# Performance work log

Hardware: AMD Instinct MI355X
Metric: run time of the kernel (lower is better)

## Reference

```python
import jax, jax.numpy as jnp
import numpy as np
from math import isqrt

NUM_HEADS = 8
EPS = 1e-12  # torch F.normalize default eps


def _l2_normalize_seq(t):
    # normalize over the sequence axis (dim=-2), matching F.normalize(t, dim=-2)
    n = jnp.sqrt(jnp.sum(t * t, axis=-2, keepdims=True))
    return t / jnp.maximum(n, EPS)


def setup_inputs() -> dict:
    key = jax.random.key(0)
    ks = jax.random.split(key, 7)
    B, L, C = 8, 4096, 384
    s = 0.02
    return {
        "x": jax.random.normal(ks[0], (B, L, C), jnp.float32),
        "qkv_w": jax.random.normal(ks[1], (3 * C, C), jnp.float32) * s,
        "qkv_b": jax.random.normal(ks[2], (3 * C,), jnp.float32) * s,
        "proj_w": jax.random.normal(ks[3], (C, C), jnp.float32) * s,
        "proj_b": jax.random.normal(ks[4], (C,), jnp.float32) * s,
        "temperature": jnp.ones((NUM_HEADS, 1, 1), jnp.float32),
        "conv_w": jax.random.normal(ks[5], (C, 1, 3, 3), jnp.float32) * s,
        "conv_b": jax.random.normal(ks[6], (C,), jnp.float32) * s,
    }


def reference(x, qkv_w, qkv_b, proj_w, proj_b, temperature, conv_w, conv_b):
    B, L, C = x.shape
    h = NUM_HEADS
    d = C // h
    H = W = isqrt(L)

    # qkv projection -> (3, B, h, L, d)
    qkv = (x @ qkv_w.T + qkv_b).reshape(B, L, 3, h, d).transpose(2, 0, 3, 1, 4)
    q, k, v = qkv[0], qkv[1], qkv[2]

    # L2 normalize q, k over sequence axis
    q = _l2_normalize_seq(q)
    k = _l2_normalize_seq(k)

    # LePE: depthwise 3x3 conv on v in image layout (B, C, H, W)
    v_img = v.transpose(0, 1, 3, 2).reshape(B, C, H, W)
    lepe = jax.lax.conv_general_dilated(
        v_img, conv_w, window_strides=(1, 1), padding=((1, 1), (1, 1)),
        feature_group_count=C,
        dimension_numbers=("NCHW", "OIHW", "NCHW"),
    ) + conv_b[None, :, None, None]
    lepe = lepe.reshape(B, h, d, L).transpose(0, 1, 3, 2)  # (B, h, L, d)

    # linear attention: attn = (k^T v) * temperature, shape (B, h, d, d)
    attn = jnp.einsum("bhld,bhle->bhde", k, v) * temperature
    out = jnp.einsum("bhld,bhde->bhle", q, attn) + lepe  # (B, h, L, d)

    out = out.transpose(0, 2, 1, 3).reshape(B, L, C)
    out = out @ proj_w.T + proj_b
    return (out, attn)
```

## Files before the change

kernel.cpp:

```cpp
#include <hip/hip_runtime.h>
#include <hip/hip_bf16.h>


typedef __bf16 bf16x8 __attribute__((ext_vector_type(8)));
typedef float f32x4 __attribute__((ext_vector_type(4)));

__device__ inline __bf16 f2b(float f) {
    __hip_bfloat16 h = __float2bfloat16(f);
    __bf16 r; __builtin_memcpy(&r, &h, 2); return r;
}
__device__ inline float b2f(__hip_bfloat16 h) { return __bfloat162float(h); }
__device__ inline float b2f(__bf16 v) {
    __hip_bfloat16 h; __builtin_memcpy(&h, &v, 2); return __bfloat162float(h);
}

__device__ inline bf16x8 load8(const __hip_bfloat16* p) {
    uint4 v = *(const uint4*)p;
    bf16x8 r; __builtin_memcpy(&r, &v, 16); return r;
}
__device__ inline bf16x8 load8(const float* p) {
    float4 a = *(const float4*)p;
    float4 b = *(const float4*)(p + 4);
    bf16x8 r;
    r[0] = f2b(a.x); r[1] = f2b(a.y); r[2] = f2b(a.z); r[3] = f2b(a.w);
    r[4] = f2b(b.x); r[5] = f2b(b.y); r[6] = f2b(b.z); r[7] = f2b(b.w);
    return r;
}

__device__ inline void storef(float* p, float v) { *p = v; }
__device__ inline void storef(__hip_bfloat16* p, float v) { *p = __float2bfloat16(v); }

__device__ inline void gl_lds16(const __hip_bfloat16* g, __hip_bfloat16* l) {
    __builtin_amdgcn_global_load_lds(
        (const __attribute__((address_space(1))) void*)g,
        (__attribute__((address_space(3))) void*)l,
        16, 0, 0);
}

__global__ __launch_bounds__(256) void cvt_kernel(
    const float* __restrict__ x,  __hip_bfloat16* __restrict__ xb,
    const float* __restrict__ qw, __hip_bfloat16* __restrict__ qwb,
    const float* __restrict__ pw, __hip_bfloat16* __restrict__ pwb,
    uint4* __restrict__ zdst)
{
    int blk = blockIdx.x;
    if (blk >= 6432) {
        zdst[(size_t)(blk - 6432) * 256 + threadIdx.x] = (uint4){0, 0, 0, 0};
        return;
    }
    const float* src; __hip_bfloat16* dst; int base;
    if (blk < 6144)      { src = x;  dst = xb;  base = blk; }
    else if (blk < 6360) { src = qw; dst = qwb; base = blk - 6144; }
    else                 { src = pw; dst = pwb; base = blk - 6360; }
    int i = base * 256 + threadIdx.x;
    bf16x8 v = load8(src + (size_t)i * 8);
    *(bf16x8*)(dst + (size_t)i * 8) = v;
}

template <typename TO, int KC, bool FUSE_SQ>
__global__ __launch_bounds__(256) void gemm_bf16_nt(
    const __hip_bfloat16* __restrict__ A,
    const __hip_bfloat16* __restrict__ Bw,
    const float* __restrict__ bias,
    TO* __restrict__ C,
    int N, int NXT,
    float* __restrict__ sq)
{
    __shared__ __hip_bfloat16 As[128 * 64];
    __shared__ __hip_bfloat16 Bs[64 * 64];
    const int t = threadIdx.x;
    const int w = t >> 6, lane = t & 63;
    const int r16 = lane & 15, quad = lane >> 4;
    const int bx  = blockIdx.x;
    const int xcd = bx & 7, seq = bx >> 3;
    const int n_t = seq % NXT, m_t = seq / NXT;
    const int m0 = (xcd + 8 * m_t) * 128;
    const int n0 = n_t * 64;
    const int wm = w >> 1, wn = w & 1;

    f32x4 acc[4][2];
    #pragma unroll
    for (int mi = 0; mi < 4; ++mi)
        #pragma unroll
        for (int ni = 0; ni < 2; ++ni)
            acc[mi][ni] = (f32x4){0.f, 0.f, 0.f, 0.f};

    for (int k0 = 0; k0 < KC; k0 += 64) {
        #pragma unroll
        for (int p = 0; p < 4; ++p) {
            int c = p * 64 + lane;
            int rl = c >> 3;
            int cc = (c & 7) ^ (rl & 7);
            gl_lds16(A + (size_t)(m0 + w * 32 + rl) * KC + k0 + cc * 8,
                     &As[(w * 256 + c) * 8]);
        }
        #pragma unroll
        for (int p = 0; p < 2; ++p) {
            int c = p * 64 + lane;
            int rl = c >> 3;
            int cc = (c & 7) ^ (rl & 7);
            gl_lds16(Bw + (size_t)(n0 + w * 16 + rl) * KC + k0 + cc * 8,
                     &Bs[(w * 128 + c) * 8]);
        }
        __syncthreads();
        bf16x8 af[4][2], bfr[2][2];
        #pragma unroll
        for (int ks = 0; ks < 2; ++ks) {
            #pragma unroll
            for (int mi = 0; mi < 4; ++mi) {
                int row = wm * 64 + mi * 16 + r16;
                int pc  = (ks * 4 + quad) ^ (r16 & 7);
                af[mi][ks] = *(const bf16x8*)&As[row * 64 + pc * 8];
            }
            #pragma unroll
            for (int ni = 0; ni < 2; ++ni) {
                int row = wn * 32 + ni * 16 + r16;
                int pc  = (ks * 4 + quad) ^ (r16 & 7);
                bfr[ni][ks] = *(const bf16x8*)&Bs[row * 64 + pc * 8];
            }
        }
        #pragma unroll
        for (int ks = 0; ks < 2; ++ks)
            #pragma unroll
            for (int mi = 0; mi < 4; ++mi)
                #pragma unroll
                for (int ni = 0; ni < 2; ++ni)
                    acc[mi][ni] = __builtin_amdgcn_mfma_f32_16x16x32_bf16(
                        af[mi][ks], bfr[ni][ks], acc[mi][ni], 0, 0, 0);
        __syncthreads();
    }

    #pragma unroll
    for (int ni = 0; ni < 2; ++ni) {
        int col = n0 + wn * 32 + ni * 16 + r16;
        float bv = bias[col];
        float s = 0.f;
        #pragma unroll
        for (int mi = 0; mi < 4; ++mi) {
            #pragma unroll
            for (int reg = 0; reg < 4; ++reg) {
                int row = m0 + wm * 64 + mi * 16 + quad * 4 + reg;
                float o = acc[mi][ni][reg] + bv;
                storef(&C[(size_t)row * N + col], o);
                s += o * o;
            }
        }
        if constexpr (FUSE_SQ) {
            if (col < 768) {
                s += __shfl_xor(s, 16);
                s += __shfl_xor(s, 32);
                if (quad == 0) {
                    int b = m0 >> 12;
                    atomicAdd(&sq[b * 768 + col], s);
                }
            }
        }
    }
}

__global__ __launch_bounds__(256) void ktv_mfma_kernel(
    const __hip_bfloat16* __restrict__ qkv, float* __restrict__ G)
{
    __shared__ __hip_bfloat16 kT[4][48][40];
    __shared__ __hip_bfloat16 vT[4][48][40];

    const int bh = blockIdx.y; const int b = bh >> 3; const int h = bh & 7;
    const int lbase = blockIdx.x * 256;
    const int t = threadIdx.x;
    const int w = t >> 6, lane = t & 63;
    const int r16 = lane & 15, quad = lane >> 4;

    f32x4 acc[3][3];
    #pragma unroll
    for (int mi = 0; mi < 3; ++mi)
        #pragma unroll
        for (int ni = 0; ni < 3; ++ni)
            acc[mi][ni] = (f32x4){0.f, 0.f, 0.f, 0.f};

    const int mat  = t & 1;
    const int lrow = t >> 1;
    const int tile = lrow >> 5, l_in = lrow & 31;
    const __hip_bfloat16* src = qkv + 384 + mat * 384 + h * 48;
    __hip_bfloat16* dstT = (mat ? &vT[0][0][0] : &kT[0][0][0]) + ((size_t)tile * 48 * 40 + l_in);

    for (int it = 0; it < 2; ++it) {
        const int l0 = lbase + it * 128;
        const __hip_bfloat16* p = src + (size_t)(b * 4096 + l0 + lrow) * 1152;
        __hip_bfloat16 row[48];
        #pragma unroll
        for (int j = 0; j < 6; ++j) {
            uint4 v = *(const uint4*)(p + j * 8);
            __builtin_memcpy(&row[j * 8], &v, 16);
        }
        #pragma unroll
        for (int d = 0; d < 48; ++d)
            dstT[d * 40] = row[d];
        __syncthreads();

        bf16x8 af[3], bfr[3];
        #pragma unroll
        for (int mi = 0; mi < 3; ++mi)
            af[mi] = *(const bf16x8*)&kT[w][mi * 16 + r16][quad * 8];
        #pragma unroll
        for (int ni = 0; ni < 3; ++ni)
            bfr[ni] = *(const bf16x8*)&vT[w][ni * 16 + r16][quad * 8];
        #pragma unroll
        for (int mi = 0; mi < 3; ++mi)
            #pragma unroll
            for (int ni = 0; ni < 3; ++ni)
                acc[mi][ni] = __builtin_amdgcn_mfma_f32_16x16x32_bf16(af[mi], bfr[ni], acc[mi][ni], 0, 0, 0);
        __syncthreads();
    }

    float* red2 = (float*)&kT[0][0][0];
    if (w >= 2) {
        #pragma unroll
        for (int mi = 0; mi < 3; ++mi)
            #pragma unroll
            for (int ni = 0; ni < 3; ++ni)
                #pragma unroll
                for (int reg = 0; reg < 4; ++reg)
                    red2[((w - 2) * 48 + mi * 16 + quad * 4 + reg) * 49 + ni * 16 + r16]
                        = acc[mi][ni][reg];
    }
    __syncthreads();
    if (w < 2) {
        float* Gb = G + (size_t)bh * 2304;
        #pragma unroll
        for (int mi = 0; mi < 3; ++mi)
            #pragma unroll
            for (int ni = 0; ni < 3; ++ni)
                #pragma unroll
                for (int reg = 0; reg < 4; ++reg) {
                    int row = mi * 16 + quad * 4 + reg;
                    int col = ni * 16 + r16;
                    float s = acc[mi][ni][reg] + red2[(w * 48 + row) * 49 + col];
                    atomicAdd(&Gb[row * 48 + col], s);
                }
    }
}

__global__ __launch_bounds__(256) void qattn_lepe_mfma(
    const __hip_bfloat16* __restrict__ qkv, const float* __restrict__ G,
    const float* __restrict__ sumsq, const float* __restrict__ temp,
    const float* __restrict__ conv_w, const float* __restrict__ conv_b,
    __hip_bfloat16* __restrict__ y, float* __restrict__ attn_out)
{
    __shared__ __attribute__((aligned(16))) char smem[26624];
    __hip_bfloat16 (*qs)[72]  = (__hip_bfloat16 (*)[72])smem;
    __hip_bfloat16 (*a2s)[72] = (__hip_bfloat16 (*)[72])(smem + 18432);
    float (*ys)[52]           = (float (*)[52])smem;
    __shared__ __hip_bfloat16 vs[4][64][48];
    __shared__ float cwT[9][48];
    __shared__ float cb[48];
    __shared__ float ink_s[48], inq_s[48];

    const int bh = blockIdx.y; const int b = bh >> 3; const int h = bh & 7;
    const int yi0 = blockIdx.x * 2;
    const int l0  = yi0 * 64;
    const int t = threadIdx.x;
    const int w = t >> 6, lane = t & 63;
    const int r16 = lane & 15, quad = lane >> 4;
    const float tf = temp[h];

    if (t < 48) {
        ink_s[t] = 1.f / fmaxf(sqrtf(sumsq[b * 768 + 384 + h * 48 + t]), 1e-12f);
        inq_s[t] = 1.f / fmaxf(sqrtf(sumsq[b * 768 +       h * 48 + t]), 1e-12f);
    }
    __syncthreads();

    const float* Gb = G + (size_t)bh * 2304;

    if (blockIdx.x == 0) {
        for (int e = t; e < 2304; e += 256)
            attn_out[(size_t)bh * 2304 + e] = Gb[e] * ink_s[e / 48] * tf;
    }

    const __hip_bfloat16* qbase = qkv + (size_t)(b * 4096 + l0) * 1152 + h * 48;
    #pragma unroll
    for (int i = 0; i < 3; ++i) {
        int chunk = t + i * 256;
        int row = chunk / 6, cg = chunk % 6;
        *(bf16x8*)&qs[row][cg * 8] = load8(qbase + (size_t)row * 1152 + cg * 8);
    }
    *(bf16x8*)&qs[t >> 1][48 + (t & 1) * 8] = (bf16x8)0;

    for (int i = t; i < 3072; i += 256) {
        int e = i >> 6, dd = i & 63;
        float val = 0.f;
        if (dd < 48) {
            float av = Gb[dd * 48 + e] * ink_s[dd] * tf;
            val = av * inq_s[dd];
        }
        a2s[e][dd] = __float2bfloat16(val);
    }

    const __hip_bfloat16* vbase = qkv + (size_t)b * 4096 * 1152 + 768 + h * 48;
    #pragma unroll
    for (int i = 0; i < 6; ++i) {
        int chunk = t + i * 256;
        int r = chunk / 384, rem = chunk % 384;
        int xx = rem / 6, cg = rem % 6;
        int yy = yi0 - 1 + r;
        bf16x8 v = (yy >= 0 && yy < 64)
            ? load8(vbase + (size_t)(yy * 64 + xx) * 1152 + cg * 8)
            : (bf16x8)0;
        *(bf16x8*)&vs[r][xx][cg * 8] = v;
    }

    for (int i = t; i < 432; i += 256)
        cwT[i / 48][i % 48] = conv_w[(h * 48 + (i % 48)) * 9 + (i / 48)];
    if (t < 48) cb[t] = conv_b[h * 48 + t];
    __syncthreads();

    f32x4 acc[2][3];
    #pragma unroll
    for (int mi = 0; mi < 2; ++mi)
        #pragma unroll
        for (int ni = 0; ni < 3; ++ni)
            acc[mi][ni] = (f32x4){0.f, 0.f, 0.f, 0.f};
    #pragma unroll
    for (int ks = 0; ks < 2; ++ks) {
        int kb = ks * 32 + quad * 8;
        bf16x8 af[2], bfr[3];
        #pragma unroll
        for (int mi = 0; mi < 2; ++mi)
            af[mi] = *(const bf16x8*)&qs[w * 32 + mi * 16 + r16][kb];
        #pragma unroll
        for (int ni = 0; ni < 3; ++ni)
            bfr[ni] = *(const bf16x8*)&a2s[ni * 16 + r16][kb];
        #pragma unroll
        for (int mi = 0; mi < 2; ++mi)
            #pragma unroll
            for (int ni = 0; ni < 3; ++ni)
                acc[mi][ni] = __builtin_amdgcn_mfma_f32_16x16x32_bf16(af[mi], bfr[ni], acc[mi][ni], 0, 0, 0);
    }
    __syncthreads();

    #pragma unroll
    for (int mi = 0; mi < 2; ++mi)
        #pragma unroll
        for (int ni = 0; ni < 3; ++ni)
            #pragma unroll
            for (int reg = 0; reg < 4; ++reg)
                ys[w * 32 + mi * 16 + quad * 4 + reg][ni * 16 + r16] = acc[mi][ni][reg];
    __syncthreads();

    __hip_bfloat16* ybase = y + (size_t)(b * 4096 + l0) * 384 + h * 48;
    #pragma unroll
    for (int i = 0; i < 3; ++i) {
        int g = t + i * 256;
        int l_in = g / 6, cg = g % 6, e0 = cg * 8;
        int xi = l_in & 63, vr0 = l_in >> 6;
        float o[8];
        #pragma unroll
        for (int j = 0; j < 8; ++j) o[j] = ys[l_in][e0 + j] + cb[e0 + j];
        #pragma unroll
        for (int dy = 0; dy < 3; ++dy) {
            #pragma unroll
            for (int dx = 0; dx < 3; ++dx) {
                int xx = xi + dx - 1;
                if (xx < 0 || xx > 63) continue;
                bf16x8 vv = *(const bf16x8*)&vs[vr0 + dy][xx][e0];
                const float* cwp = &cwT[dy * 3 + dx][e0];
                #pragma unroll
                for (int j = 0; j < 8; ++j) o[j] += b2f(vv[j]) * cwp[j];
            }
        }
        __hip_bfloat16 ob[8];
        #pragma unroll
        for (int j = 0; j < 8; ++j) ob[j] = __float2bfloat16(o[j]);
        uint4 pk; __builtin_memcpy(&pk, ob, 16);
        *(uint4*)(ybase + (size_t)l_in * 384 + e0) = pk;
    }
}

extern "C" void kernel_launch(void* const* d_in, const int* in_sizes, int n_in,
                              void* d_out, int out_size, void* d_ws, size_t ws_size,
                              hipStream_t stream)
{
    const float* x      = (const float*)d_in[0];
    const float* qkv_w  = (const float*)d_in[1];
    const float* qkv_b  = (const float*)d_in[2];
    const float* proj_w = (const float*)d_in[3];
    const float* proj_b = (const float*)d_in[4];
    const float* temp   = (const float*)d_in[5];
    const float* conv_w = (const float*)d_in[6];
    const float* conv_b = (const float*)d_in[7];

    char* ws = (char*)d_ws;
    __hip_bfloat16* qkv = (__hip_bfloat16*)(ws);
    __hip_bfloat16* yb  = (__hip_bfloat16*)(ws + 75497472);
    float* sumsq = (float*)(ws + 100663296);
    float* G     = (float*)(ws + 100687872);
    __hip_bfloat16* x_bf16  = yb;
    __hip_bfloat16* qkv_wb  = (__hip_bfloat16*)(ws + 101892096);
    __hip_bfloat16* proj_wb = (__hip_bfloat16*)(ws + 102776832);

    float* out      = (float*)d_out;
    float* attn_out = out + 12582912;

    cvt_kernel<<<6582, 256, 0, stream>>>(x, x_bf16, qkv_w, qkv_wb, proj_w, proj_wb,
                                         (uint4*)(ws + 100663296));
    gemm_bf16_nt<__hip_bfloat16, 384, true><<<4608, 256, 0, stream>>>(
        x_bf16, qkv_wb, qkv_b, qkv, 1152, 18, sumsq);
    ktv_mfma_kernel<<<dim3(16, 64), 256, 0, stream>>>(qkv, G);
    qattn_lepe_mfma<<<dim3(32, 64), 256, 0, stream>>>(
        qkv, G, sumsq, temp, conv_w, conv_b, yb, attn_out);
    gemm_bf16_nt<float, 384, false><<<1536, 256, 0, stream>>>(
        yb, proj_wb, proj_b, out, 384, 6, nullptr);
}
```

Before: 227.2 us.

## Restructure linear attention via per-batch Gram matrix and folded effective weights

```diff
diff --git a/kernel.cpp b/kernel.cpp
--- a/kernel.cpp
+++ b/kernel.cpp
@@ -57,14 +57,499 @@
     *(bf16x8*)(dst + (size_t)i * 8) = v;
 }
 
-template <typename TO, int KC, bool FUSE_SQ>
+__global__ __launch_bounds__(256) void xpose_kernel(
+    const __hip_bfloat16* __restrict__ xb, __hip_bfloat16* __restrict__ xT,
+    float* __restrict__ m)
+{
+    __shared__ __hip_bfloat16 tile[64][72];
+    const int lt = blockIdx.x, ct = blockIdx.y, b = blockIdx.z;
+    const int l0 = lt * 64, c0 = ct * 64;
+    const int t = threadIdx.x;
+
+    #pragma unroll
+    for (int p = 0; p < 2; ++p) {
+        int cid = t + p * 256;
+        int row = cid >> 3, ch = cid & 7;
+        *(bf16x8*)&tile[row][ch * 8] =
+            load8(xb + (size_t)(b * 4096 + l0 + row) * 384 + c0 + ch * 8);
+    }
+    __syncthreads();
+
+    #pragma unroll
+    for (int p = 0; p < 2; ++p) {
+        int ocid = t + p * 256;
+        int c = ocid >> 3, lch = ocid & 7;
+        __hip_bfloat16 vals[8];
+        #pragma unroll
+        for (int k = 0; k < 8; ++k) {
+            int j = (k + lch) & 7;
+            vals[j] = tile[lch * 8 + j][c];
+        }
+        bf16x8 pk;
+        float s = 0.f;
+        #pragma unroll
+        for (int j = 0; j < 8; ++j) { pk[j] = *(__bf16*)&vals[j]; s += b2f(vals[j]); }
+        *(bf16x8*)(xT + ((size_t)b * 384 + c0 + c) * 4096 + l0 + lch * 8) = pk;
+        s += __shfl_xor(s, 1); s += __shfl_xor(s, 2); s += __shfl_xor(s, 4);
+        if ((ocid & 7) == 0) atomicAdd(&m[b * 384 + c0 + c], s);
+    }
+}
+
+__global__ __launch_bounds__(256) void syrk_part(
+    const __hip_bfloat16* __restrict__ xT, float* __restrict__ Spart)
+{
+    __shared__ __hip_bfloat16 As[128 * 64];
+    __shared__ __hip_bfloat16 Bs[64 * 64];
+    const int t = threadIdx.x;
+    const int w = t >> 6, lane = t & 63;
+    const int r16 = lane & 15, quad = lane >> 4;
+    const int bx = blockIdx.x;
+    const int b = bx / 72, rem = bx % 72;
+    const int tile = rem / 4, split = rem % 4;
+    const int m0 = (tile / 6) * 128, n0 = (tile % 6) * 64;
+    const int k_lo = split * 1024;
+    const int wm = w >> 1, wn = w & 1;
+    const __hip_bfloat16* A = xT + (size_t)b * 384 * 4096;
+
+    f32x4 acc[4][2];
+    #pragma unroll
+    for (int mi = 0; mi < 4; ++mi)
+        #pragma unroll
+        for (int ni = 0; ni < 2; ++ni)
+            acc[mi][ni] = (f32x4){0.f, 0.f, 0.f, 0.f};
+
+    for (int it = 0; it < 16; ++it) {
+        const int k0 = k_lo + it * 64;
+        #pragma unroll
+        for (int p = 0; p < 4; ++p) {
+            int c = p * 64 + lane;
+            int rl = c >> 3;
+            int cc = (c & 7) ^ (rl & 7);
+            gl_lds16(A + (size_t)(m0 + w * 32 + rl) * 4096 + k0 + cc * 8,
+                     &As[(w * 256 + c) * 8]);
+        }
+        #pragma unroll
+        for (int p = 0; p < 2; ++p) {
+            int c = p * 64 + lane;
+            int rl = c >> 3;
+            int cc = (c & 7) ^ (rl & 7);
+            gl_lds16(A + (size_t)(n0 + w * 16 + rl) * 4096 + k0 + cc * 8,
+                     &Bs[(w * 128 + c) * 8]);
+        }
+        __syncthreads();
+        bf16x8 af[4][2], bfr[2][2];
+        #pragma unroll
+        for (int ks = 0; ks < 2; ++ks) {
+            #pragma unroll
+            for (int mi = 0; mi < 4; ++mi) {
+                int row = wm * 64 + mi * 16 + r16;
+                int pc  = (ks * 4 + quad) ^ (r16 & 7);
+                af[mi][ks] = *(const bf16x8*)&As[row * 64 + pc * 8];
+            }
+            #pragma unroll
+            for (int ni = 0; ni < 2; ++ni) {
+                int row = wn * 32 + ni * 16 + r16;
+                int pc  = (ks * 4 + quad) ^ (r16 & 7);
+                bfr[ni][ks] = *(const bf16x8*)&Bs[row * 64 + pc * 8];
+            }
+        }
+        #pragma unroll
+        for (int ks = 0; ks < 2; ++ks)
+            #pragma unroll
+            for (int mi = 0; mi < 4; ++mi)
+                #pragma unroll
+                for (int ni = 0; ni < 2; ++ni)
+                    acc[mi][ni] = __builtin_amdgcn_mfma_f32_16x16x32_bf16(
+                        af[mi][ks], bfr[ni][ks], acc[mi][ni], 0, 0, 0);
+        __syncthreads();
+    }
+
+    float* outp = Spart + (size_t)(split * 8 + b) * 147456;
+    #pragma unroll
+    for (int ni = 0; ni < 2; ++ni) {
+        int col = n0 + wn * 32 + ni * 16 + r16;
+        #pragma unroll
+        for (int mi = 0; mi < 4; ++mi)
+            #pragma unroll
+            for (int reg = 0; reg < 4; ++reg) {
+                int row = m0 + wm * 64 + mi * 16 + quad * 4 + reg;
+                outp[(size_t)row * 384 + col] = acc[mi][ni][reg];
+            }
+    }
+}
+
+__global__ __launch_bounds__(256) void cvtS_kernel(
+    const float* __restrict__ Spart, __hip_bfloat16* __restrict__ S2)
+{
+    size_t base = ((size_t)blockIdx.x * 256 + threadIdx.x) * 8;
+    int b = (int)(base / 147456);
+    size_t off = base % 147456;
+    float s[8];
+    #pragma unroll
+    for (int j = 0; j < 8; ++j) s[j] = 0.f;
+    #pragma unroll
+    for (int sp = 0; sp < 4; ++sp) {
+        const float* p = Spart + (size_t)(sp * 8 + b) * 147456 + off;
+        float4 a = *(const float4*)p, c = *(const float4*)(p + 4);
+        s[0] += a.x; s[1] += a.y; s[2] += a.z; s[3] += a.w;
+        s[4] += c.x; s[5] += c.y; s[6] += c.z; s[7] += c.w;
+    }
+    bf16x8 hi, lo;
+    #pragma unroll
+    for (int j = 0; j < 8; ++j) {
+        __hip_bfloat16 h = __float2bfloat16(s[j]);
+        hi[j] = *(__bf16*)&h;
+        __hip_bfloat16 l2 = __float2bfloat16(s[j] - __bfloat162float(h));
+        lo[j] = *(__bf16*)&l2;
+    }
+    *(bf16x8*)(S2 + (size_t)(b * 2 + 0) * 147456 + off) = hi;
+    *(bf16x8*)(S2 + (size_t)(b * 2 + 1) * 147456 + off) = lo;
+}
+
+__global__ __launch_bounds__(256) void gemm_T(
+    const __hip_bfloat16* __restrict__ Wqk, const __hip_bfloat16* __restrict__ S2,
+    float* __restrict__ T)
+{
+    __shared__ __hip_bfloat16 As[128 * 64];
+    __shared__ __hip_bfloat16 Bs[64 * 64];
+    const int t = threadIdx.x;
+    const int w = t >> 6, lane = t & 63;
+    const int r16 = lane & 15, quad = lane >> 4;
+    const int bx = blockIdx.x;
+    const int b = bx / 36, rem = bx % 36;
+    const int m0 = (rem / 6) * 128, n0 = (rem % 6) * 64;
+    const int wm = w >> 1, wn = w & 1;
+
+    f32x4 acc[4][2];
+    #pragma unroll
+    for (int mi = 0; mi < 4; ++mi)
+        #pragma unroll
+        for (int ni = 0; ni < 2; ++ni)
+            acc[mi][ni] = (f32x4){0.f, 0.f, 0.f, 0.f};
+
+    for (int pass = 0; pass < 2; ++pass) {
+        const __hip_bfloat16* Bw = S2 + (size_t)(b * 2 + pass) * 147456;
+        for (int k0 = 0; k0 < 384; k0 += 64) {
+            #pragma unroll
+            for (int p = 0; p < 4; ++p) {
+                int c = p * 64 + lane;
+                int rl = c >> 3;
+                int cc = (c & 7) ^ (rl & 7);
+                gl_lds16(Wqk + (size_t)(m0 + w * 32 + rl) * 384 + k0 + cc * 8,
+                         &As[(w * 256 + c) * 8]);
+            }
+            #pragma unroll
+            for (int p = 0; p < 2; ++p) {
+                int c = p * 64 + lane;
+                int rl = c >> 3;
+                int cc = (c & 7) ^ (rl & 7);
+                gl_lds16(Bw + (size_t)(n0 + w * 16 + rl) * 384 + k0 + cc * 8,
+                         &Bs[(w * 128 + c) * 8]);
+            }
+            __syncthreads();
+            bf16x8 af[4][2], bfr[2][2];
+            #pragma unroll
+            for (int ks = 0; ks < 2; ++ks) {
+                #pragma unroll
+                for (int mi = 0; mi < 4; ++mi) {
+                    int row = wm * 64 + mi * 16 + r16;
+                    int pc  = (ks * 4 + quad) ^ (r16 & 7);
+                    af[mi][ks] = *(const bf16x8*)&As[row * 64 + pc * 8];
+                }
+                #pragma unroll
+                for (int ni = 0; ni < 2; ++ni) {
+                    int row = wn * 32 + ni * 16 + r16;
+                    int pc  = (ks * 4 + quad) ^ (r16 & 7);
+                    bfr[ni][ks] = *(const bf16x8*)&Bs[row * 64 + pc * 8];
+                }
+            }
+            #pragma unroll
+            for (int ks = 0; ks < 2; ++ks)
+                #pragma unroll
+                for (int mi = 0; mi < 4; ++mi)
+                    #pragma unroll
+                    for (int ni = 0; ni < 2; ++ni)
+                        acc[mi][ni] = __builtin_amdgcn_mfma_f32_16x16x32_bf16(
+                            af[mi][ks], bfr[ni][ks], acc[mi][ni], 0, 0, 0);
+            __syncthreads();
+        }
+    }
+
+    float* Cp = T + (size_t)b * 768 * 384;
+    #pragma unroll
+    for (int ni = 0; ni < 2; ++ni) {
+        int col = n0 + wn * 32 + ni * 16 + r16;
+        #pragma unroll
+        for (int mi = 0; mi < 4; ++mi)
+            #pragma unroll
+            for (int reg = 0; reg < 4; ++reg) {
+                int row = m0 + wm * 64 + mi * 16 + quad * 4 + reg;
+                Cp[(size_t)row * 384 + col] = acc[mi][ni][reg];
+            }
+    }
+}
+
+__global__ __launch_bounds__(256) void head_kernel(
+    const float* __restrict__ T, const float* __restrict__ m,
+    const __hip_bfloat16* __restrict__ qkvw, const float* __restrict__ qkv_b,
+    const float* __restrict__ temp,
+    float* __restrict__ attn_out, __hip_bfloat16* __restrict__ weff,
+    float* __restrict__ beff)
+{
+    __shared__ __hip_bfloat16 wlds[48][384];
+    __shared__ float A2[48][48];
+    __shared__ float ink[48], inq[48], kbm[48], vbm[48], qbm[48];
+    __shared__ float bk_s[48], bv_s[48], bq_s[48];
+
+    const int bh = blockIdx.x; const int b = bh >> 3, h = bh & 7;
+    const int t = threadIdx.x;
+    const float tf = temp[h];
+    const float* mb = m + b * 384;
+    const float* tq = T + ((size_t)b * 768 + h * 48) * 384;
+    const float* tk = T + ((size_t)b * 768 + 384 + h * 48) * 384;
+
+    for (int i = t; i < 48 * 48; i += 256) {
+        int r = i / 48, c = i % 48;
+        *(bf16x8*)&wlds[r][c * 8] = load8(qkvw + (size_t)(768 + h * 48 + r) * 384 + c * 8);
+    }
+    if (t < 48) {
+        bq_s[t] = qkv_b[h * 48 + t];
+        bk_s[t] = qkv_b[384 + h * 48 + t];
+        bv_s[t] = qkv_b[768 + h * 48 + t];
+    }
+    if (t < 144) {
+        int kind = t / 48, d = t % 48;
+        int rbase = (kind == 0) ? 384 + h * 48 + d : (kind == 1) ? 768 + h * 48 + d : h * 48 + d;
+        const __hip_bfloat16* wr = qkvw + (size_t)rbase * 384;
+        float s = 0.f;
+        for (int j0 = 0; j0 < 384; j0 += 8) {
+            bf16x8 wv = load8(wr + j0);
+            const float4 a = *(const float4*)(mb + j0);
+            const float4 c = *(const float4*)(mb + j0 + 4);
+            s += b2f(wv[0])*a.x + b2f(wv[1])*a.y + b2f(wv[2])*a.z + b2f(wv[3])*a.w
+               + b2f(wv[4])*c.x + b2f(wv[5])*c.y + b2f(wv[6])*c.z + b2f(wv[7])*c.w;
+        }
+        if (kind == 0) kbm[d] = s; else if (kind == 1) vbm[d] = s; else qbm[d] = s;
+    }
+    __syncthreads();
+
+    if (t < 96) {
+        int d = t % 48; bool isq = t >= 48;
+        const float* trow = (isq ? tq : tk) + (size_t)d * 384;
+        const __hip_bfloat16* wr = qkvw + (size_t)((isq ? 0 : 384) + h * 48 + d) * 384;
+        float bb = isq ? bq_s[d] : bk_s[d];
+        float s = 0.f;
+        for (int j0 = 0; j0 < 384; j0 += 8) {
+            bf16x8 wv = load8(wr + j0);
+            const float4 a = *(const float4*)(trow + j0);
+            const float4 c = *(const float4*)(trow + j0 + 4);
+            s += a.x*b2f(wv[0]) + a.y*b2f(wv[1]) + a.z*b2f(wv[2]) + a.w*b2f(wv[3])
+               + c.x*b2f(wv[4]) + c.y*b2f(wv[5]) + c.z*b2f(wv[6]) + c.w*b2f(wv[7]);
+        }
+        s += 2.f * bb * (isq ? qbm[d] : kbm[d]) + 4096.f * bb * bb;
+        float r = 1.f / fmaxf(sqrtf(s), 1e-12f);
+        if (isq) inq[d] = r; else ink[d] = r;
+    }
+    __syncthreads();
+
+    #pragma unroll
+    for (int kk = 0; kk < 9; ++kk) {
+        int cell = t + kk * 256;
+        int d = cell / 48, e = cell % 48;
+        const float* trow = tk + (size_t)d * 384;
+        float g = 0.f;
+        for (int j0 = 0; j0 < 384; j0 += 8) {
+            bf16x8 wv = *(const bf16x8*)&wlds[e][j0];
+            const float4 a = *(const float4*)(trow + j0);
+            const float4 c = *(const float4*)(trow + j0 + 4);
+            g += a.x*b2f(wv[0]) + a.y*b2f(wv[1]) + a.z*b2f(wv[2]) + a.w*b2f(wv[3])
+               + c.x*b2f(wv[4]) + c.y*b2f(wv[5]) + c.z*b2f(wv[6]) + c.w*b2f(wv[7]);
+        }
+        g += kbm[d] * bv_s[e] + bk_s[d] * vbm[e] + 4096.f * bk_s[d] * bv_s[e];
+        float av = g * ink[d] * tf;
+        attn_out[(size_t)bh * 2304 + cell] = av;
+        A2[d][e] = av * inq[d];
+    }
+    __syncthreads();
+
+    for (int i = t; i < 48 * 48; i += 256) {
+        int r = i / 48, c = i % 48;
+        *(bf16x8*)&wlds[r][c * 8] = load8(qkvw + (size_t)(h * 48 + r) * 384 + c * 8);
+    }
+    if (t < 48) {
+        float s = 0.f;
+        #pragma unroll
+        for (int d2 = 0; d2 < 48; ++d2) s += bq_s[d2] * A2[d2][t];
+        beff[(size_t)b * 384 + h * 48 + t] = s;
+    }
+    __syncthreads();
+
+    for (int idx = t; idx < 48 * 384; idx += 256) {
+        int e = idx / 384, i2 = idx % 384;
+        float s = 0.f;
+        #pragma unroll
+        for (int d2 = 0; d2 < 48; ++d2) s += A2[d2][e] * b2f(wlds[d2][i2]);
+        weff[((size_t)b * 384 + h * 48 + e) * 384 + i2] = __float2bfloat16(s);
+    }
+}
+
+__global__ __launch_bounds__(256) void gemm_vy(
+    const __hip_bfloat16* __restrict__ A, const __hip_bfloat16* __restrict__ qkvw,
+    const __hip_bfloat16* __restrict__ weff,
+    const float* __restrict__ qkv_b, const float* __restrict__ beff,
+    __hip_bfloat16* __restrict__ C)
+{
+    __shared__ __hip_bfloat16 As[128 * 64];
+    __shared__ __hip_bfloat16 Bs[64 * 64];
+    const int t = threadIdx.x;
+    const int w = t >> 6, lane = t & 63;
+    const int r16 = lane & 15, quad = lane >> 4;
+    const int bx = blockIdx.x;
+    const int xcd = bx & 7, seq = bx >> 3;
+    const int n_t = seq % 12, m_t = seq / 12;
+    const int m0 = (xcd + 8 * m_t) * 128;
+    const int n0 = n_t * 64;
+    const int b = m0 >> 12;
+    const int wm = w >> 1, wn = w & 1;
+
+    f32x4 acc[4][2];
+    #pragma unroll
+    for (int mi = 0; mi < 4; ++mi)
+        #pragma unroll
+        for (int ni = 0; ni < 2; ++ni)
+            acc[mi][ni] = (f32x4){0.f, 0.f, 0.f, 0.f};
+
+    for (int k0 = 0; k0 < 384; k0 += 64) {
+        #pragma unroll
+        for (int p = 0; p < 4; ++p) {
+            int c = p * 64 + lane;
+            int rl = c >> 3;
+            int cc = (c & 7) ^ (rl & 7);
+            gl_lds16(A + (size_t)(m0 + w * 32 + rl) * 384 + k0 + cc * 8,
+                     &As[(w * 256 + c) * 8]);
+        }
+        #pragma unroll
+        for (int p = 0; p < 2; ++p) {
+            int c = p * 64 + lane;
+            int rl = c >> 3;
+            int cc = (c & 7) ^ (rl & 7);
+            int n = n0 + w * 16 + rl;
+            const __hip_bfloat16* brow = (n < 384)
+                ? qkvw + (size_t)(768 + n) * 384
+                : weff + ((size_t)b * 384 + (n - 384)) * 384;
+            gl_lds16(brow + k0 + cc * 8, &Bs[(w * 128 + c) * 8]);
+        }
+        __syncthreads();
+        bf16x8 af[4][2], bfr[2][2];
+        #pragma unroll
+        for (int ks = 0; ks < 2; ++ks) {
+            #pragma unroll
+            for (int mi = 0; mi < 4; ++mi) {
+                int row = wm * 64 + mi * 16 + r16;
+                int pc  = (ks * 4 + quad) ^ (r16 & 7);
+                af[mi][ks] = *(const bf16x8*)&As[row * 64 + pc * 8];
+            }
+            #pragma unroll
+            for (int ni = 0; ni < 2; ++ni) {
+                int row = wn * 32 + ni * 16 + r16;
+                int pc  = (ks * 4 + quad) ^ (r16 & 7);
+                bfr[ni][ks] = *(const bf16x8*)&Bs[row * 64 + pc * 8];
+            }
+        }
+        #pragma unroll
+        for (int ks = 0; ks < 2; ++ks)
+            #pragma unroll
+            for (int mi = 0; mi < 4; ++mi)
+                #pragma unroll
+                for (int ni = 0; ni < 2; ++ni)
+                    acc[mi][ni] = __builtin_amdgcn_mfma_f32_16x16x32_bf16(
+                        af[mi][ks], bfr[ni][ks], acc[mi][ni], 0, 0, 0);
+        __syncthreads();
+    }
+
+    #pragma unroll
+    for (int ni = 0; ni < 2; ++ni) {
+        int col = n0 + wn * 32 + ni * 16 + r16;
+        float bv = (col < 384) ? qkv_b[768 + col] : beff[(size_t)b * 384 + col - 384];
+        #pragma unroll
+        for (int mi = 0; mi < 4; ++mi)
+            #pragma unroll
+            for (int reg = 0; reg < 4; ++reg) {
+                int row = m0 + wm * 64 + mi * 16 + quad * 4 + reg;
+                C[(size_t)row * 768 + col] = __float2bfloat16(acc[mi][ni][reg] + bv);
+            }
+    }
+}
+
+__global__ __launch_bounds__(256) void lepe_kernel(
+    const __hip_bfloat16* __restrict__ vy,
+    const float* __restrict__ conv_w, const float* __restrict__ conv_b,
+    __hip_bfloat16* __restrict__ y)
+{
+    __shared__ __hip_bfloat16 vs[4][64][48];
+    __shared__ float cwT[9][48];
+    __shared__ float cb[48];
+
+    const int bh = blockIdx.y; const int b = bh >> 3; const int h = bh & 7;
+    const int yi0 = blockIdx.x * 2;
+    const int l0  = yi0 * 64;
+    const int t = threadIdx.x;
+
+    const __hip_bfloat16* vbase = vy + (size_t)b * 4096 * 768 + h * 48;
+    #pragma unroll
+    for (int i = 0; i < 6; ++i) {
+        int chunk = t + i * 256;
+        int r = chunk / 384, rem = chunk % 384;
+        int xx = rem / 6, cg = rem % 6;
+        int yy = yi0 - 1 + r;
+        bf16x8 v = (yy >= 0 && yy < 64)
+            ? load8(vbase + (size_t)(yy * 64 + xx) * 768 + cg * 8)
+            : (bf16x8)0;
+        *(bf16x8*)&vs[r][xx][cg * 8] = v;
+    }
+    for (int i = t; i < 432; i += 256)
+        cwT[i / 48][i % 48] = conv_w[(h * 48 + (i % 48)) * 9 + (i / 48)];
+    if (t < 48) cb[t] = conv_b[h * 48 + t];
+    __syncthreads();
+
+    const __hip_bfloat16* ybase_in = vy + (size_t)(b * 4096 + l0) * 768 + 384 + h * 48;
+    __hip_bfloat16* ybase = y + (size_t)(b * 4096 + l0) * 384 + h * 48;
+    #pragma unroll
+    for (int i = 0; i < 3; ++i) {
+        int g = t + i * 256;
+        int l_in = g / 6, cg = g % 6, e0 = cg * 8;
+        int xi = l_in & 63, vr0 = l_in >> 6;
+        bf16x8 yp = load8(ybase_in + (size_t)l_in * 768 + e0);
+        float o[8];
+        #pragma unroll
+        for (int j = 0; j < 8; ++j) o[j] = b2f(yp[j]) + cb[e0 + j];
+        #pragma unroll
+        for (int dy = 0; dy < 3; ++dy) {
+            #pragma unroll
+            for (int dx = 0; dx < 3; ++dx) {
+                int xx = xi + dx - 1;
+                if (xx < 0 || xx > 63) continue;
+                bf16x8 vv = *(const bf16x8*)&vs[vr0 + dy][xx][e0];
+                const float* cwp = &cwT[dy * 3 + dx][e0];
+                #pragma unroll
+                for (int j = 0; j < 8; ++j) o[j] += b2f(vv[j]) * cwp[j];
+            }
+        }
+        __hip_bfloat16 ob[8];
+        #pragma unroll
+        for (int j = 0; j < 8; ++j) ob[j] = __float2bfloat16(o[j]);
+        uint4 pk; __builtin_memcpy(&pk, ob, 16);
+        *(uint4*)(ybase + (size_t)l_in * 384 + e0) = pk;
+    }
+}
+
+template <typename TO, int KC>
 __global__ __launch_bounds__(256) void gemm_bf16_nt(
     const __hip_bfloat16* __restrict__ A,
     const __hip_bfloat16* __restrict__ Bw,
     const float* __restrict__ bias,
     TO* __restrict__ C,
-    int N, int NXT,
-    float* __restrict__ sq)
+    int N, int NXT)
 {
     __shared__ __hip_bfloat16 As[128 * 64];
     __shared__ __hip_bfloat16 Bs[64 * 64];
@@ -134,244 +619,13 @@
     for (int ni = 0; ni < 2; ++ni) {
         int col = n0 + wn * 32 + ni * 16 + r16;
         float bv = bias[col];
-        float s = 0.f;
-        #pragma unroll
-        for (int mi = 0; mi < 4; ++mi) {
+        #pragma unroll
+        for (int mi = 0; mi < 4; ++mi)
             #pragma unroll
             for (int reg = 0; reg < 4; ++reg) {
                 int row = m0 + wm * 64 + mi * 16 + quad * 4 + reg;
-                float o = acc[mi][ni][reg] + bv;
-                storef(&C[(size_t)row * N + col], o);
-                s += o * o;
-            }
-        }
-        if constexpr (FUSE_SQ) {
-            if (col < 768) {
-                s += __shfl_xor(s, 16);
-                s += __shfl_xor(s, 32);
-                if (quad == 0) {
-                    int b = m0 >> 12;
-                    atomicAdd(&sq[b * 768 + col], s);
-                }
-            }
-        }
-    }
-}
-
-__global__ __launch_bounds__(256) void ktv_mfma_kernel(
-    const __hip_bfloat16* __restrict__ qkv, float* __restrict__ G)
-{
-    __shared__ __hip_bfloat16 kT[4][48][40];
-    __shared__ __hip_bfloat16 vT[4][48][40];
-
-    const int bh = blockIdx.y; const int b = bh >> 3; const int h = bh & 7;
-    const int lbase = blockIdx.x * 256;
-    const int t = threadIdx.x;
-    const int w = t >> 6, lane = t & 63;
-    const int r16 = lane & 15, quad = lane >> 4;
-
-    f32x4 acc[3][3];
-    #pragma unroll
-    for (int mi = 0; mi < 3; ++mi)
-        #pragma unroll
-        for (int ni = 0; ni < 3; ++ni)
-            acc[mi][ni] = (f32x4){0.f, 0.f, 0.f, 0.f};
-
-    const int mat  = t & 1;
-    const int lrow = t >> 1;
-    const int tile = lrow >> 5, l_in = lrow & 31;
-    const __hip_bfloat16* src = qkv + 384 + mat * 384 + h * 48;
-    __hip_bfloat16* dstT = (mat ? &vT[0][0][0] : &kT[0][0][0]) + ((size_t)tile * 48 * 40 + l_in);
-
-    for (int it = 0; it < 2; ++it) {
-        const int l0 = lbase + it * 128;
-        const __hip_bfloat16* p = src + (size_t)(b * 4096 + l0 + lrow) * 1152;
-        __hip_bfloat16 row[48];
-        #pragma unroll
-        for (int j = 0; j < 6; ++j) {
-            uint4 v = *(const uint4*)(p + j * 8);
-            __builtin_memcpy(&row[j * 8], &v, 16);
-        }
-        #pragma unroll
-        for (int d = 0; d < 48; ++d)
-            dstT[d * 40] = row[d];
-        __syncthreads();
-
-        bf16x8 af[3], bfr[3];
-        #pragma unroll
-        for (int mi = 0; mi < 3; ++mi)
-            af[mi] = *(const bf16x8*)&kT[w][mi * 16 + r16][quad * 8];
-        #pragma unroll
-        for (int ni = 0; ni < 3; ++ni)
-            bfr[ni] = *(const bf16x8*)&vT[w][ni * 16 + r16][quad * 8];
-        #pragma unroll
-        for (int mi = 0; mi < 3; ++mi)
-            #pragma unroll
-            for (int ni = 0; ni < 3; ++ni)
-                acc[mi][ni] = __builtin_amdgcn_mfma_f32_16x16x32_bf16(af[mi], bfr[ni], acc[mi][ni], 0, 0, 0);
-        __syncthreads();
-    }
-
-    float* red2 = (float*)&kT[0][0][0];
-    if (w >= 2) {
-        #pragma unroll
-        for (int mi = 0; mi < 3; ++mi)
-            #pragma unroll
-            for (int ni = 0; ni < 3; ++ni)
-                #pragma unroll
-                for (int reg = 0; reg < 4; ++reg)
-                    red2[((w - 2) * 48 + mi * 16 + quad * 4 + reg) * 49 + ni * 16 + r16]
-                        = acc[mi][ni][reg];
-    }
-    __syncthreads();
-    if (w < 2) {
-        float* Gb = G + (size_t)bh * 2304;
-        #pragma unroll
-        for (int mi = 0; mi < 3; ++mi)
-            #pragma unroll
-            for (int ni = 0; ni < 3; ++ni)
-                #pragma unroll
-                for (int reg = 0; reg < 4; ++reg) {
-                    int row = mi * 16 + quad * 4 + reg;
-                    int col = ni * 16 + r16;
-                    float s = acc[mi][ni][reg] + red2[(w * 48 + row) * 49 + col];
-                    atomicAdd(&Gb[row * 48 + col], s);
-                }
-    }
-}
-
-__global__ __launch_bounds__(256) void qattn_lepe_mfma(
-    const __hip_bfloat16* __restrict__ qkv, const float* __restrict__ G,
-    const float* __restrict__ sumsq, const float* __restrict__ temp,
-    const float* __restrict__ conv_w, const float* __restrict__ conv_b,
-    __hip_bfloat16* __restrict__ y, float* __restrict__ attn_out)
-{
-    __shared__ __attribute__((aligned(16))) char smem[26624];
-    __hip_bfloat16 (*qs)[72]  = (__hip_bfloat16 (*)[72])smem;
-    __hip_bfloat16 (*a2s)[72] = (__hip_bfloat16 (*)[72])(smem + 18432);
-    float (*ys)[52]           = (float (*)[52])smem;
-    __shared__ __hip_bfloat16 vs[4][64][48];
-    __shared__ float cwT[9][48];
-    __shared__ float cb[48];
-    __shared__ float ink_s[48], inq_s[48];
-
-    const int bh = blockIdx.y; const int b = bh >> 3; const int h = bh & 7;
-    const int yi0 = blockIdx.x * 2;
-    const int l0  = yi0 * 64;
-    const int t = threadIdx.x;
-    const int w = t >> 6, lane = t & 63;
-    const int r16 = lane & 15, quad = lane >> 4;
-    const float tf = temp[h];
-
-    if (t < 48) {
-        ink_s[t] = 1.f / fmaxf(sqrtf(sumsq[b * 768 + 384 + h * 48 + t]), 1e-12f);
-        inq_s[t] = 1.f / fmaxf(sqrtf(sumsq[b * 768 +       h * 48 + t]), 1e-12f);
-    }
-    __syncthreads();
-
-    const float* Gb = G + (size_t)bh * 2304;
-
-    if (blockIdx.x == 0) {
-        for (int e = t; e < 2304; e += 256)
-            attn_out[(size_t)bh * 2304 + e] = Gb[e] * ink_s[e / 48] * tf;
-    }
-
-    const __hip_bfloat16* qbase = qkv + (size_t)(b * 4096 + l0) * 1152 + h * 48;
-    #pragma unroll
-    for (int i = 0; i < 3; ++i) {
-        int chunk = t + i * 256;
-        int row = chunk / 6, cg = chunk % 6;
-        *(bf16x8*)&qs[row][cg * 8] = load8(qbase + (size_t)row * 1152 + cg * 8);
-    }
-    *(bf16x8*)&qs[t >> 1][48 + (t & 1) * 8] = (bf16x8)0;
-
-    for (int i = t; i < 3072; i += 256) {
-        int e = i >> 6, dd = i & 63;
-        float val = 0.f;
-        if (dd < 48) {
-            float av = Gb[dd * 48 + e] * ink_s[dd] * tf;
-            val = av * inq_s[dd];
-        }
-        a2s[e][dd] = __float2bfloat16(val);
-    }
-
-    const __hip_bfloat16* vbase = qkv + (size_t)b * 4096 * 1152 + 768 + h * 48;
-    #pragma unroll
-    for (int i = 0; i < 6; ++i) {
-        int chunk = t + i * 256;
-        int r = chunk / 384, rem = chunk % 384;
-        int xx = rem / 6, cg = rem % 6;
-        int yy = yi0 - 1 + r;
-        bf16x8 v = (yy >= 0 && yy < 64)
-            ? load8(vbase + (size_t)(yy * 64 + xx) * 1152 + cg * 8)
-            : (bf16x8)0;
-        *(bf16x8*)&vs[r][xx][cg * 8] = v;
-    }
-
-    for (int i = t; i < 432; i += 256)
-        cwT[i / 48][i % 48] = conv_w[(h * 48 + (i % 48)) * 9 + (i / 48)];
-    if (t < 48) cb[t] = conv_b[h * 48 + t];
-    __syncthreads();
-
-    f32x4 acc[2][3];
-    #pragma unroll
-    for (int mi = 0; mi < 2; ++mi)
-        #pragma unroll
-        for (int ni = 0; ni < 3; ++ni)
-            acc[mi][ni] = (f32x4){0.f, 0.f, 0.f, 0.f};
-    #pragma unroll
-    for (int ks = 0; ks < 2; ++ks) {
-        int kb = ks * 32 + quad * 8;
-        bf16x8 af[2], bfr[3];
-        #pragma unroll
-        for (int mi = 0; mi < 2; ++mi)
-            af[mi] = *(const bf16x8*)&qs[w * 32 + mi * 16 + r16][kb];
-        #pragma unroll
-        for (int ni = 0; ni < 3; ++ni)
-            bfr[ni] = *(const bf16x8*)&a2s[ni * 16 + r16][kb];
-        #pragma unroll
-        for (int mi = 0; mi < 2; ++mi)
-            #pragma unroll
-            for (int ni = 0; ni < 3; ++ni)
-                acc[mi][ni] = __builtin_amdgcn_mfma_f32_16x16x32_bf16(af[mi], bfr[ni], acc[mi][ni], 0, 0, 0);
-    }
-    __syncthreads();
-
-    #pragma unroll
-    for (int mi = 0; mi < 2; ++mi)
-        #pragma unroll
-        for (int ni = 0; ni < 3; ++ni)
-            #pragma unroll
-            for (int reg = 0; reg < 4; ++reg)
-                ys[w * 32 + mi * 16 + quad * 4 + reg][ni * 16 + r16] = acc[mi][ni][reg];
-    __syncthreads();
-
-    __hip_bfloat16* ybase = y + (size_t)(b * 4096 + l0) * 384 + h * 48;
-    #pragma unroll
-    for (int i = 0; i < 3; ++i) {
-        int g = t + i * 256;
-        int l_in = g / 6, cg = g % 6, e0 = cg * 8;
-        int xi = l_in & 63, vr0 = l_in >> 6;
-        float o[8];
-        #pragma unroll
-        for (int j = 0; j < 8; ++j) o[j] = ys[l_in][e0 + j] + cb[e0 + j];
-        #pragma unroll
-        for (int dy = 0; dy < 3; ++dy) {
-            #pragma unroll
-            for (int dx = 0; dx < 3; ++dx) {
-                int xx = xi + dx - 1;
-                if (xx < 0 || xx > 63) continue;
-                bf16x8 vv = *(const bf16x8*)&vs[vr0 + dy][xx][e0];
-                const float* cwp = &cwT[dy * 3 + dx][e0];
-                #pragma unroll
-                for (int j = 0; j < 8; ++j) o[j] += b2f(vv[j]) * cwp[j];
-            }
-        }
-        __hip_bfloat16 ob[8];
-        #pragma unroll
-        for (int j = 0; j < 8; ++j) ob[j] = __float2bfloat16(o[j]);
-        uint4 pk; __builtin_memcpy(&pk, ob, 16);
-        *(uint4*)(ybase + (size_t)l_in * 384 + e0) = pk;
+                storef(&C[(size_t)row * N + col], acc[mi][ni][reg] + bv);
+            }
     }
 }
 
@@ -389,24 +643,32 @@
     const float* conv_b = (const float*)d_in[7];
 
     char* ws = (char*)d_ws;
-    __hip_bfloat16* qkv = (__hip_bfloat16*)(ws);
-    __hip_bfloat16* yb  = (__hip_bfloat16*)(ws + 75497472);
-    float* sumsq = (float*)(ws + 100663296);
-    float* G     = (float*)(ws + 100687872);
-    __hip_bfloat16* x_bf16  = yb;
-    __hip_bfloat16* qkv_wb  = (__hip_bfloat16*)(ws + 101892096);
-    __hip_bfloat16* proj_wb = (__hip_bfloat16*)(ws + 102776832);
+    __hip_bfloat16* vy   = (__hip_bfloat16*)(ws);
+    __hip_bfloat16* xT   = (__hip_bfloat16*)(ws);
+    __hip_bfloat16* xb   = (__hip_bfloat16*)(ws + 50331648);
+    __hip_bfloat16* yb   = (__hip_bfloat16*)(ws + 50331648);
+    float* Spart         = (float*)(ws + 75497472);
+    float* T             = (float*)(ws + 75497472);
+    __hip_bfloat16* weff = (__hip_bfloat16*)(ws + 84934656);
+    float* beff          = (float*)(ws + 87293952);
+    __hip_bfloat16* S2   = (__hip_bfloat16*)(ws + 94371840);
+    float* m             = (float*)(ws + 99090432);
+    __hip_bfloat16* qkv_wb  = (__hip_bfloat16*)(ws + 99102720);
+    __hip_bfloat16* proj_wb = (__hip_bfloat16*)(ws + 99987456);
 
     float* out      = (float*)d_out;
     float* attn_out = out + 12582912;
 
-    cvt_kernel<<<6582, 256, 0, stream>>>(x, x_bf16, qkv_w, qkv_wb, proj_w, proj_wb,
-                                         (uint4*)(ws + 100663296));
-    gemm_bf16_nt<__hip_bfloat16, 384, true><<<4608, 256, 0, stream>>>(
-        x_bf16, qkv_wb, qkv_b, qkv, 1152, 18, sumsq);
-    ktv_mfma_kernel<<<dim3(16, 64), 256, 0, stream>>>(qkv, G);
-    qattn_lepe_mfma<<<dim3(32, 64), 256, 0, stream>>>(
-        qkv, G, sumsq, temp, conv_w, conv_b, yb, attn_out);
-    gemm_bf16_nt<float, 384, false><<<1536, 256, 0, stream>>>(
-        yb, proj_wb, proj_b, out, 384, 6, nullptr);
-}
+    cvt_kernel<<<6435, 256, 0, stream>>>(x, xb, qkv_w, qkv_wb, proj_w, proj_wb,
+                                         (uint4*)m);
+    xpose_kernel<<<dim3(64, 6, 8), 256, 0, stream>>>(xb, xT, m);
+    syrk_part<<<576, 256, 0, stream>>>(xT, Spart);
+    cvtS_kernel<<<576, 256, 0, stream>>>(Spart, S2);
+    gemm_T<<<288, 256, 0, stream>>>(qkv_wb, S2, T);
+    head_kernel<<<64, 256, 0, stream>>>(T, m, qkv_wb, qkv_b, temp,
+                                        attn_out, weff, beff);
+    gemm_vy<<<3072, 256, 0, stream>>>(xb, qkv_wb, weff, qkv_b, beff, vy);
+    lepe_kernel<<<dim3(32, 64), 256, 0, stream>>>(vy, conv_w, conv_b, yb);
+    gemm_bf16_nt<float, 384><<<1536, 256, 0, stream>>>(
+        yb, proj_wb, proj_b, out, 384, 6);
+}
```

Result: slower. 415.6 us (+82.9%).
